# Performance work log

Measured on AMD Instinct MI355X. Metric: run time of the kernel, lower is better.

The kernel has to match this reference:

```python
import jax, jax.numpy as jnp
import numpy as np

B, N, DIM, H, HD, COND, BS = 2, 1024, 768, 12, 64, 128, 16
S = 2 * N  # noised tokens [0:N) concatenated with clean x0 tokens [N:2N)
EPS = 1e-5
NEG = -1e30


def setup_inputs() -> dict:
    key = jax.random.key(0)
    ks = jax.random.split(key, 8)
    d = {}
    d['x'] = jax.random.normal(ks[0], (B, S, DIM), jnp.float32)
    d['c'] = jax.random.normal(ks[1], (B, COND), jnp.float32)
    # Rotary table for positions 0..N-1 (each half of the 2N sequence reuses the same positions)
    inv_freq = 1.0 / (10000.0 ** (np.arange(0, HD, 2, dtype=np.float64) / HD))
    freqs = np.arange(N, dtype=np.float64)[:, None] * inv_freq[None, :]
    emb = np.concatenate([freqs, freqs], axis=-1)  # [N, HD]
    cos = np.tile(np.cos(emb), (2, 1))[None, :, None, None, :]
    sin = np.tile(np.sin(emb), (2, 1))[None, :, None, None, :]
    d['cos'] = jnp.asarray(cos, jnp.float32)
    d['sin'] = jnp.asarray(sin, jnp.float32)
    # block-causal diffusion mask (flex_attention_mask): same (block, x0-flag) OR
    # cross-attention from noised block q>0 to strictly earlier CLEAN (x0) blocks
    idx = np.arange(S)
    fl = (idx >= N).astype(np.int64)
    blk = np.where(fl == 1, (idx - N) // BS, idx // BS)
    same = (blk[:, None] == blk[None, :]) & (fl[:, None] == fl[None, :])
    allowed = (blk[:, None] > 0) & (blk[None, :] < blk[:, None]) & (fl[None, :] == 1)
    d['mask'] = jnp.asarray(same | allowed)
    # parameters (adaLN is zero-init in the source; randomized here so the block is non-trivial)
    w = 0.02
    d['norm1_w'] = jnp.ones((DIM,), jnp.float32)
    d['qkv_w'] = jax.random.normal(ks[2], (3 * DIM, DIM), jnp.float32) * w
    d['attn_out_w'] = jax.random.normal(ks[3], (DIM, DIM), jnp.float32) * w
    d['norm2_w'] = jnp.ones((DIM,), jnp.float32)
    d['mlp_w1'] = jax.random.normal(ks[4], (4 * DIM, DIM), jnp.float32) * w
    d['mlp_b1'] = jnp.zeros((4 * DIM,), jnp.float32)
    d['mlp_w2'] = jax.random.normal(ks[5], (DIM, 4 * DIM), jnp.float32) * w
    d['mlp_b2'] = jnp.zeros((DIM,), jnp.float32)
    d['adaLN_w'] = jax.random.normal(ks[6], (6 * DIM, COND), jnp.float32) * w
    d['adaLN_b'] = jax.random.normal(ks[7], (6 * DIM,), jnp.float32) * w
    return d


def _ln(x, w):
    # F.layer_norm (no bias) followed by learned scale, as in the custom LayerNorm
    mu = x.mean(-1, keepdims=True)
    xc = x - mu
    var = (xc * xc).mean(-1, keepdims=True)
    return xc * jax.lax.rsqrt(var + EPS) * w


def reference(x, c, cos, sin, mask, norm1_w, qkv_w, attn_out_w, norm2_w,
              mlp_w1, mlp_b1, mlp_w2, mlp_b2, adaLN_w, adaLN_b):
    # adaLN modulation: [B, 6*DIM] -> six [B, 1, DIM] chunks
    mods = c @ adaLN_w.T + adaLN_b
    (shift_msa, scale_msa, gate_msa,
     shift_mlp, scale_mlp, gate_mlp) = jnp.split(mods[:, None, :], 6, axis=-1)
    x_skip = x
    h = _ln(x, norm1_w) * (1.0 + scale_msa) + shift_msa  # modulate_fused
    # qkv projection + rotary (torchscript path: qkv*cos + rotate_half(qkv)*sin)
    qkv = (h @ qkv_w.T).reshape(x.shape[0], S, 3, H, HD)
    rot = jnp.concatenate([-qkv[..., HD // 2:], qkv[..., :HD // 2]], axis=-1)
    qkv = qkv * cos + rot * sin
    q, k, v = qkv[:, :, 0], qkv[:, :, 1], qkv[:, :, 2]
    # SDPA with the block-causal diffusion mask, scale 1/sqrt(head_dim)
    scores = jnp.einsum('bqhd,bkhd->bhqk', q, k) / np.sqrt(HD).astype(np.float32)
    scores = jnp.where(mask[None, None], scores, NEG)
    p = jax.nn.softmax(scores, axis=-1)
    a = jnp.einsum('bhqk,bkhd->bqhd', p, v).reshape(x.shape[0], S, DIM)
    # bias_dropout_add_scale (inference => no dropout): gate * attn_out + residual
    x = gate_msa * (a @ attn_out_w.T) + x_skip
    h2 = _ln(x, norm2_w) * (1.0 + scale_mlp) + shift_mlp
    m = jax.nn.gelu(h2 @ mlp_w1.T + mlp_b1, approximate=True) @ mlp_w2.T + mlp_b2
    return x + gate_mlp * m
```

## Files before the change

kernel.cpp:

```cpp
#include <hip/hip_runtime.h>
#include <hip/hip_bf16.h>

#define EPS 1e-5f

typedef __attribute__((ext_vector_type(8))) short bf16x8;
typedef __attribute__((ext_vector_type(4))) short bf16x4;
typedef __attribute__((ext_vector_type(4))) float f32x4;

__device__ __forceinline__ f32x4 mfma_bf16(bf16x8 a, bf16x8 b, f32x4 c) {
    return __builtin_amdgcn_mfma_f32_16x16x32_bf16(a, b, c, 0, 0, 0);
}

__device__ __forceinline__ void async_ld16(const void* g, void* l) {
    __builtin_amdgcn_global_load_lds(
        (const __attribute__((address_space(1))) void*)g,
        (__attribute__((address_space(3))) void*)l, 16, 0, 0);
}

__device__ __forceinline__ float fast_gelu(float v) {
    float z2 = 1.5957691216057308f * (v + 0.044715f * v * v * v);
    float e = __expf(z2);
    return v * e / (e + 1.f);
}

__device__ __forceinline__ float bf2f(short s) {
    union { float f; unsigned u; } v;
    v.u = ((unsigned)(unsigned short)s) << 16;
    return v.f;
}

__global__ void k_pre(const float* __restrict__ a, __hip_bfloat16* __restrict__ oa, int na,
                      const float* __restrict__ b, __hip_bfloat16* __restrict__ ob, int nb,
                      const float* __restrict__ c, __hip_bfloat16* __restrict__ oc, int nc,
                      const float* __restrict__ d, __hip_bfloat16* __restrict__ od, int nd,
                      const float* __restrict__ cond, const float* __restrict__ alw,
                      const float* __restrict__ alb, float* __restrict__ mods) {
    if (blockIdx.x >= 27648) {
        int i = (blockIdx.x - 27648) * 256 + threadIdx.x;
        int bb = i / 4608, row = i - bb * 4608;
        const float4* cv = (const float4*)(cond + bb * 128);
        const float4* wv = (const float4*)(alw + (long)row * 128);
        float acc = 0.f;
#pragma unroll
        for (int k = 0; k < 32; ++k) {
            float4 x = cv[k], y = wv[k];
            acc += x.x * y.x + x.y * y.y + x.z * y.z + x.w * y.w;
        }
        mods[i] = acc + alb[row];
        return;
    }
    int i = blockIdx.x * 256 + threadIdx.x;
    if (i < na) { oa[i] = __float2bfloat16(a[i]); return; }
    i -= na;
    if (i < nb) { ob[i] = __float2bfloat16(b[i]); return; }
    i -= nb;
    if (i < nc) { oc[i] = __float2bfloat16(c[i]); return; }
    i -= nc;
    if (i < nd) od[i] = __float2bfloat16(d[i]);
}

__global__ void k_ln_mod(const float* __restrict__ x, const float* __restrict__ w,
                         const float* __restrict__ mods, int shiftOff, int scaleOff,
                         __hip_bfloat16* __restrict__ out) {
    int token = blockIdx.x;
    int lane = threadIdx.x;
    const float4* xr = (const float4*)(x + (long)token * 768);
    float4 v0 = xr[lane], v1 = xr[lane + 64], v2 = xr[lane + 128];
    float s  = v0.x + v0.y + v0.z + v0.w + v1.x + v1.y + v1.z + v1.w + v2.x + v2.y + v2.z + v2.w;
    float ss = v0.x*v0.x + v0.y*v0.y + v0.z*v0.z + v0.w*v0.w
             + v1.x*v1.x + v1.y*v1.y + v1.z*v1.z + v1.w*v1.w
             + v2.x*v2.x + v2.y*v2.y + v2.z*v2.z + v2.w*v2.w;
#pragma unroll
    for (int m = 32; m >= 1; m >>= 1) { s += __shfl_xor(s, m); ss += __shfl_xor(ss, m); }
    float mu = s * (1.f / 768.f);
    float var = ss * (1.f / 768.f) - mu * mu;
    float rs = rsqrtf(var + EPS);
    int b = token >> 11;
    const float* sh = mods + b * 4608 + shiftOff;
    const float* sc = mods + b * 4608 + scaleOff;
    __hip_bfloat16* o = out + (long)token * 768;
    float4 vv[3] = {v0, v1, v2};
#pragma unroll
    for (int kk = 0; kk < 3; ++kk) {
        int cbase = (lane + 64 * kk) * 4;
        const float* p = (const float*)&vv[kk];
#pragma unroll
        for (int j = 0; j < 4; ++j) {
            int col = cbase + j;
            float hv = (p[j] - mu) * rs * w[col] * (1.f + sc[col]) + sh[col];
            o[col] = __float2bfloat16(hv);
        }
    }
}

__global__ void k_red(const __hip_bfloat16* __restrict__ p, const float* __restrict__ x2,
                      const float* __restrict__ mods, const float* __restrict__ bias,
                      float* __restrict__ out) {
    long base = ((long)blockIdx.x * 256 + threadIdx.x) * 4;
    int col = (int)(base % 768);
    int row = (int)(base / 768);
    int b = row >> 11;
    short4 a0 = *(const short4*)(p + base);
    short4 a1 = *(const short4*)(p + 3145728 + base);
    float4 xr = *(const float4*)(x2 + base);
    float4 gt = *(const float4*)(mods + b * 4608 + 3840 + col);
    float4 bs = *(const float4*)(bias + col);
    float4 o;
    o.x = xr.x + gt.x * (bf2f(a0.x) + bf2f(a1.x) + bs.x);
    o.y = xr.y + gt.y * (bf2f(a0.y) + bf2f(a1.y) + bs.y);
    o.z = xr.z + gt.z * (bf2f(a0.z) + bf2f(a1.z) + bs.z);
    o.w = xr.w + gt.w * (bf2f(a0.w) + bf2f(a1.w) + bs.w);
    *(float4*)(out + base) = o;
}

__global__ __launch_bounds__(64) void k_attn(
    const __hip_bfloat16* __restrict__ q, const __hip_bfloat16* __restrict__ k,
    const __hip_bfloat16* __restrict__ vT, __hip_bfloat16* __restrict__ out) {
    __shared__ __hip_bfloat16 P[640];
    int lane = threadIdx.x;
    int l15 = lane & 15, quad = lane >> 4;
    int idx = blockIdx.x;
    int bh = idx % 24;
    int r = idx / 24;
    int fl, blk;
    if (r & 1) { fl = 1; blk = 63 - (r >> 1); }
    else       { fl = 0; blk = 63 - (r >> 1); }
    int qblk = fl * 64 + blk;

    const __hip_bfloat16* Q = q + ((long)bh * 2048 + qblk * 16) * 64;
    bf16x8 qa = *(const bf16x8*)(Q + l15 * 64 + quad * 8);
    bf16x8 qb = *(const bf16x8*)(Q + l15 * 64 + 32 + quad * 8);
    const __hip_bfloat16* K = k + (long)bh * 2048 * 64;
    const __hip_bfloat16* V = vT + (long)bh * 64 * 2048;

    const f32x4 vzero = {0.f, 0.f, 0.f, 0.f};
    f32x4 o[4]; float l[4];
#pragma unroll
    for (int rr = 0; rr < 4; ++rr) { o[rr] = vzero; l[rr] = 0.f; }

    int plen = (blk + fl) * 16;
    int nch = (plen + 31) >> 5;
    int total = nch + (fl ? 0 : 1);

    int kbase = (0 < nch) ? 1024 : blk * 16;
    bool v1 = (0 < nch) && (16 < plen);
    bf16x8 ka, kb, k1a, k1b;
    {
        const __hip_bfloat16* K0 = K + (long)kbase * 64;
        ka = *(const bf16x8*)(K0 + l15 * 64 + quad * 8);
        kb = *(const bf16x8*)(K0 + l15 * 64 + 32 + quad * 8);
        k1a = ka; k1b = kb;
        if (v1) {
            const __hip_bfloat16* K1 = K0 + 16 * 64;
            k1a = *(const bf16x8*)(K1 + l15 * 64 + quad * 8);
            k1b = *(const bf16x8*)(K1 + l15 * 64 + 32 + quad * 8);
        }
    }

    for (int ci = 0; ci < total; ++ci) {
        bf16x8 vf[4];
#pragma unroll
        for (int tt = 0; tt < 4; ++tt)
            vf[tt] = *(const bf16x8*)(V + (long)(tt * 16 + l15) * 2048 + kbase + quad * 8);

        f32x4 s0 = mfma_bf16(qb, kb, mfma_bf16(qa, ka, vzero));
        f32x4 s1 = vzero;
        if (v1) s1 = mfma_bf16(qb, k1b, mfma_bf16(qa, k1a, vzero));

        bool hasNext = (ci + 1) < total;
        int nkbase = kbase; bool nv1 = false;
        bf16x8 nka = ka, nkb = kb, nk1a = ka, nk1b = kb;
        if (hasNext) {
            nkbase = (ci + 1 < nch) ? 1024 + (ci + 1) * 32 : blk * 16;
            nv1 = (ci + 1 < nch) && ((ci + 1) * 32 + 16) < plen;
            const __hip_bfloat16* K0 = K + (long)nkbase * 64;
            nka = *(const bf16x8*)(K0 + l15 * 64 + quad * 8);
            nkb = *(const bf16x8*)(K0 + l15 * 64 + 32 + quad * 8);
            if (nv1) {
                const __hip_bfloat16* K1 = K0 + 16 * 64;
                nk1a = *(const bf16x8*)(K1 + l15 * 64 + quad * 8);
                nk1b = *(const bf16x8*)(K1 + l15 * 64 + 32 + quad * 8);
            }
        }

        float p0[4], p1[4];
#pragma unroll
        for (int rr = 0; rr < 4; ++rr) p0[rr] = __expf(s0[rr]);
        if (v1) {
#pragma unroll
            for (int rr = 0; rr < 4; ++rr) p1[rr] = __expf(s1[rr]);
        } else {
#pragma unroll
            for (int rr = 0; rr < 4; ++rr) p1[rr] = 0.f;
        }
#pragma unroll
        for (int rr = 0; rr < 4; ++rr) {
            l[rr] += p0[rr] + p1[rr];
            int row = quad * 4 + rr;
            P[row * 36 + l15]      = __float2bfloat16(p0[rr]);
            P[row * 36 + 16 + l15] = __float2bfloat16(p1[rr]);
        }
        asm volatile("s_waitcnt lgkmcnt(0)" ::: "memory");
        union { bf16x4 h[2]; bf16x8 v; } u;
        u.h[0] = *(const bf16x4*)(P + l15 * 36 + quad * 8);
        u.h[1] = *(const bf16x4*)(P + l15 * 36 + quad * 8 + 4);
        bf16x8 pa = u.v;
#pragma unroll
        for (int tt = 0; tt < 4; ++tt) o[tt] = mfma_bf16(pa, vf[tt], o[tt]);
        asm volatile("s_waitcnt lgkmcnt(0)" ::: "memory");

        kbase = nkbase; v1 = nv1;
        ka = nka; kb = nkb; k1a = nk1a; k1b = nk1b;
    }

    int b = bh / 12, h = bh - b * 12;
    int seqbase = qblk * 16;
#pragma unroll
    for (int rr = 0; rr < 4; ++rr) {
        float lr = l[rr];
#pragma unroll
        for (int msk = 1; msk < 16; msk <<= 1) lr += __shfl_xor(lr, msk, 16);
        float inv = 1.f / lr;
        long row = b * 2048 + seqbase + quad * 4 + rr;
#pragma unroll
        for (int tt = 0; tt < 4; ++tt)
            out[row * 768 + h * 64 + tt * 16 + l15] = __float2bfloat16(o[tt][rr] * inv);
    }
}

template <int MODE, int TN>
__global__ __launch_bounds__(TN == 128 ? 256 : 128) void k_gemm(
    const __hip_bfloat16* __restrict__ A, const __hip_bfloat16* __restrict__ W,
    float* __restrict__ Cf, __hip_bfloat16* __restrict__ Cb,
    const float* __restrict__ bias, const float* __restrict__ mods, int gateOff,
    const float* __restrict__ resid, const float* __restrict__ cosb,
    const float* __restrict__ sinb, __hip_bfloat16* __restrict__ qo,
    __hip_bfloat16* __restrict__ ko, __hip_bfloat16* __restrict__ vo,
    int M, int N, int K, int lda) {
    constexpr int NW = (TN == 128) ? 4 : 2;
    constexpr int ACH = 512 / (NW * 64);
    constexpr int BCH = (TN * 4) / (NW * 64);
    constexpr int NINST = ACH + BCH;
    __shared__ __hip_bfloat16 lA[2][128 * 32];
    __shared__ __hip_bfloat16 lB[2][TN * 32];
    int t = threadIdx.x;
    int wave = t >> 6, lane = t & 63, l15 = lane & 15, quad = lane >> 4;
    int wr = (TN == 128) ? (wave >> 1) : wave;
    int wc = (TN == 128) ? (wave & 1) : 0;
    int sw8 = (quad ^ ((l15 >> 1) & 3)) * 8;
    long bm = blockIdx.x, bn = blockIdx.y;
    const __hip_bfloat16* Ab = A + bm * 128 * lda + (long)blockIdx.z * K;
    const __hip_bfloat16* Wb = W + bn * TN * lda + (long)blockIdx.z * K;

    long soffA[ACH], soffB[BCH];
#pragma unroll
    for (int cc = 0; cc < ACH; ++cc) {
        int chunk = cc * NW * 64 + t;
        int row = chunk >> 2;
        int c = (chunk & 3) ^ ((row >> 1) & 3);
        soffA[cc] = (long)row * lda + c * 8;
    }
#pragma unroll
    for (int cc = 0; cc < BCH; ++cc) {
        int chunk = cc * NW * 64 + t;
        int row = chunk >> 2;
        int c = (chunk & 3) ^ ((row >> 1) & 3);
        soffB[cc] = (long)row * lda + c * 8;
    }
    auto stage = [&](int k0, int buf) {
        char* lAc = (char*)&lA[buf][0];
        char* lBc = (char*)&lB[buf][0];
#pragma unroll
        for (int cc = 0; cc < ACH; ++cc)
            async_ld16(Ab + soffA[cc] + k0, lAc + cc * (NW * 1024) + wave * 1024);
#pragma unroll
        for (int cc = 0; cc < BCH; ++cc)
            async_ld16(Wb + soffB[cc] + k0, lBc + cc * (NW * 1024) + wave * 1024);
    };

    f32x4 acc[4][4];
#pragma unroll
    for (int i = 0; i < 4; ++i)
#pragma unroll
        for (int j = 0; j < 4; ++j) acc[i][j] = (f32x4){0.f, 0.f, 0.f, 0.f};

    int nIter = K / 32;
    stage(0, 0);
    for (int i = 0; i < nIter; ++i) {
        int cb = i & 1;
        if (i > 0) asm volatile("s_barrier" ::: "memory");
        if (i + 1 < nIter) {
            stage((i + 1) * 32, cb ^ 1);
            asm volatile("s_waitcnt vmcnt(%0)" :: "n"(NINST) : "memory");
        } else {
            asm volatile("s_waitcnt vmcnt(0)" ::: "memory");
        }
        asm volatile("s_barrier" ::: "memory");
        bf16x8 af[4], bfr[4];
#pragma unroll
        for (int ii = 0; ii < 4; ++ii)
            af[ii] = *(const bf16x8*)&lA[cb][(wr * 64 + ii * 16 + l15) * 32 + sw8];
#pragma unroll
        for (int j = 0; j < 4; ++j)
            bfr[j] = *(const bf16x8*)&lB[cb][(wc * 64 + j * 16 + l15) * 32 + sw8];
#pragma unroll
        for (int ii = 0; ii < 4; ++ii)
#pragma unroll
            for (int j = 0; j < 4; ++j)
                acc[ii][j] = mfma_bf16(af[ii], bfr[j], acc[ii][j]);
    }

    if (MODE == 4) {
        int hcol = (int)bn * 2 + wc;
        int th = hcol / 12, h = hcol % 12;
#pragma unroll
        for (int i = 0; i < 4; ++i) {
#pragma unroll
            for (int r = 0; r < 4; ++r) {
                int row = (int)bm * 128 + wr * 64 + i * 16 + quad * 4 + r;
                int s = row & 2047, b = row >> 11;
                long bh_ = b * 12 + h;
                const float* cbp = cosb + s * 64;
                const float* sbp = sinb + s * 64;
#pragma unroll
                for (int j = 0; j < 2; ++j) {
                    int dh = j * 16 + l15;
                    float a0f = acc[i][j][r], a1f = acc[i][j + 2][r];
                    float o0 = a0f * cbp[dh] - a1f * sbp[dh];
                    float o1 = a1f * cbp[dh + 32] + a0f * sbp[dh + 32];
                    if (th == 0) {
                        __hip_bfloat16* d = qo + (bh_ * 2048 + s) * 64;
                        d[dh]      = __float2bfloat16(o0 * 0.125f);
                        d[dh + 32] = __float2bfloat16(o1 * 0.125f);
                    } else if (th == 1) {
                        __hip_bfloat16* d = ko + (bh_ * 2048 + s) * 64;
                        d[dh]      = __float2bfloat16(o0);
                        d[dh + 32] = __float2bfloat16(o1);
                    } else {
                        __hip_bfloat16* d = vo + bh_ * 64 * 2048 + s;
                        d[(long)dh * 2048]        = __float2bfloat16(o0);
                        d[(long)(dh + 32) * 2048] = __float2bfloat16(o1);
                    }
                }
            }
        }
        return;
    }

#pragma unroll
    for (int i = 0; i < 4; ++i) {
#pragma unroll
        for (int j = 0; j < 4; ++j) {
#pragma unroll
            for (int r = 0; r < 4; ++r) {
                int row = (int)bm * 128 + wr * 64 + i * 16 + quad * 4 + r;
                int col = (int)bn * TN + wc * 64 + j * 16 + l15;
                float v = acc[i][j][r];
                long idx = (long)row * N + col;
                if (MODE == 1) {
                    Cf[idx] = mods[(row >> 11) * 4608 + gateOff + col] * v + resid[idx];
                } else if (MODE == 2) {
                    Cb[idx] = __float2bfloat16(fast_gelu(v + bias[col]));
                } else if (MODE == 3) {
                    Cf[idx] = resid[idx] + mods[(row >> 11) * 4608 + gateOff + col] * (v + bias[col]);
                } else {
                    Cb[(long)blockIdx.z * M * N + idx] = __float2bfloat16(v);
                }
            }
        }
    }
}

extern "C" void kernel_launch(void* const* d_in, const int* in_sizes, int n_in,
                              void* d_out, int out_size, void* d_ws, size_t ws_size,
                              hipStream_t stream) {
    const float* x    = (const float*)d_in[0];
    const float* c    = (const float*)d_in[1];
    const float* cosb = (const float*)d_in[2];
    const float* sinb = (const float*)d_in[3];
    const float* n1w  = (const float*)d_in[5];
    const float* qkvw = (const float*)d_in[6];
    const float* aow  = (const float*)d_in[7];
    const float* n2w  = (const float*)d_in[8];
    const float* w1   = (const float*)d_in[9];
    const float* b1   = (const float*)d_in[10];
    const float* w2   = (const float*)d_in[11];
    const float* b2   = (const float*)d_in[12];
    const float* alw  = (const float*)d_in[13];
    const float* alb  = (const float*)d_in[14];

    char* ws = (char*)d_ws;
    size_t off = 0;
    auto alloc = [&](size_t bytes) -> void* {
        void* p = ws + off;
        off += (bytes + 255) & ~(size_t)255;
        return p;
    };
    float*          mods = (float*)alloc(2 * 4608 * 4);
    __hip_bfloat16* hbuf = (__hip_bfloat16*)alloc((size_t)4096 * 768 * 2);
    __hip_bfloat16* qb   = (__hip_bfloat16*)alloc((size_t)24 * 2048 * 64 * 2);
    __hip_bfloat16* kb   = (__hip_bfloat16*)alloc((size_t)24 * 2048 * 64 * 2);
    __hip_bfloat16* vT   = (__hip_bfloat16*)alloc((size_t)24 * 64 * 2048 * 2);
    __hip_bfloat16* abuf = (__hip_bfloat16*)alloc((size_t)4096 * 768 * 2);
    float*          x2   = (float*)alloc((size_t)4096 * 768 * 4);
    __hip_bfloat16* h2   = (__hip_bfloat16*)alloc((size_t)4096 * 768 * 2);
    __hip_bfloat16* m1   = (__hip_bfloat16*)alloc((size_t)4096 * 3072 * 2);
    __hip_bfloat16* m2p  = (__hip_bfloat16*)alloc((size_t)2 * 4096 * 768 * 2);
    __hip_bfloat16* wq   = (__hip_bfloat16*)alloc((size_t)2304 * 768 * 2);
    __hip_bfloat16* wa   = (__hip_bfloat16*)alloc((size_t)768 * 768 * 2);
    __hip_bfloat16* w1b  = (__hip_bfloat16*)alloc((size_t)3072 * 768 * 2);
    __hip_bfloat16* w2b  = (__hip_bfloat16*)alloc((size_t)768 * 3072 * 2);

    k_pre<<<27684, 256, 0, stream>>>(qkvw, wq, 2304 * 768, aow, wa, 768 * 768,
                                     w1, w1b, 3072 * 768, w2, w2b, 768 * 3072,
                                     c, alw, alb, mods);
    k_ln_mod<<<4096, 64, 0, stream>>>(x, n1w, mods, 0, 768, hbuf);
    k_gemm<4, 128><<<dim3(32, 18), 256, 0, stream>>>(hbuf, wq, nullptr, nullptr, nullptr, nullptr, 0,
                                                     nullptr, cosb, sinb, qb, kb, vT,
                                                     4096, 2304, 768, 768);
    k_attn<<<3072, 64, 0, stream>>>(qb, kb, vT, abuf);
    k_gemm<1, 64><<<dim3(32, 12), 128, 0, stream>>>(abuf, wa, x2, nullptr, nullptr, mods, 1536,
                                                    x, nullptr, nullptr, nullptr, nullptr, nullptr,
                                                    4096, 768, 768, 768);
    k_ln_mod<<<4096, 64, 0, stream>>>(x2, n2w, mods, 2304, 3072, h2);
    k_gemm<2, 128><<<dim3(32, 24), 256, 0, stream>>>(h2, w1b, nullptr, m1, b1, nullptr, 0,
                                                     nullptr, nullptr, nullptr, nullptr, nullptr, nullptr,
                                                     4096, 3072, 768, 768);
    k_gemm<5, 128><<<dim3(32, 6, 2), 256, 0, stream>>>(m1, w2b, nullptr, m2p, nullptr, nullptr, 0,
                                                       nullptr, nullptr, nullptr, nullptr, nullptr, nullptr,
                                                       4096, 768, 1536, 3072);
    k_red<<<3072, 256, 0, stream>>>(m2p, x2, mods, b2, (float*)d_out);
}
```

Baseline: 316.4 us.

## Process four 16-key tiles per attention iteration with per-tile key gathering

The attention loop now handles up to four 16-key tiles per iteration instead of a 32-key chunk, addressing each tile independently. The clean-prefix tiles and the diagonal self-block can therefore share one iteration, and the V fragments are gathered per tile. This cuts loop iterations, LDS round-trips and barriers per key, and gives the scheduler more independent MFMAs to overlap, at the cost of higher register use and wasted work on inactive padding tiles.

```diff
diff --git a/kernel.cpp b/kernel.cpp
--- a/kernel.cpp
+++ b/kernel.cpp
@@ -116,7 +116,7 @@
 __global__ __launch_bounds__(64) void k_attn(
     const __hip_bfloat16* __restrict__ q, const __hip_bfloat16* __restrict__ k,
     const __hip_bfloat16* __restrict__ vT, __hip_bfloat16* __restrict__ out) {
-    __shared__ __hip_bfloat16 P[640];
+    __shared__ __hip_bfloat16 P[16 * 68];
     int lane = threadIdx.x;
     int l15 = lane & 15, quad = lane >> 4;
     int idx = blockIdx.x;
@@ -139,78 +139,88 @@
     for (int rr = 0; rr < 4; ++rr) { o[rr] = vzero; l[rr] = 0.f; }
 
     int plen = (blk + fl) * 16;
-    int nch = (plen + 31) >> 5;
-    int total = nch + (fl ? 0 : 1);
-
-    int kbase = (0 < nch) ? 1024 : blk * 16;
-    bool v1 = (0 < nch) && (16 < plen);
-    bf16x8 ka, kb, k1a, k1b;
-    {
-        const __hip_bfloat16* K0 = K + (long)kbase * 64;
-        ka = *(const bf16x8*)(K0 + l15 * 64 + quad * 8);
-        kb = *(const bf16x8*)(K0 + l15 * 64 + 32 + quad * 8);
-        k1a = ka; k1b = kb;
-        if (v1) {
-            const __hip_bfloat16* K1 = K0 + 16 * 64;
-            k1a = *(const bf16x8*)(K1 + l15 * 64 + quad * 8);
-            k1b = *(const bf16x8*)(K1 + l15 * 64 + 32 + quad * 8);
-        }
-    }
-
-    for (int ci = 0; ci < total; ++ci) {
-        bf16x8 vf[4];
-#pragma unroll
-        for (int tt = 0; tt < 4; ++tt)
-            vf[tt] = *(const bf16x8*)(V + (long)(tt * 16 + l15) * 2048 + kbase + quad * 8);
-
-        f32x4 s0 = mfma_bf16(qb, kb, mfma_bf16(qa, ka, vzero));
-        f32x4 s1 = vzero;
-        if (v1) s1 = mfma_bf16(qb, k1b, mfma_bf16(qa, k1a, vzero));
-
-        bool hasNext = (ci + 1) < total;
-        int nkbase = kbase; bool nv1 = false;
-        bf16x8 nka = ka, nkb = kb, nk1a = ka, nk1b = kb;
-        if (hasNext) {
-            nkbase = (ci + 1 < nch) ? 1024 + (ci + 1) * 32 : blk * 16;
-            nv1 = (ci + 1 < nch) && ((ci + 1) * 32 + 16) < plen;
-            const __hip_bfloat16* K0 = K + (long)nkbase * 64;
-            nka = *(const bf16x8*)(K0 + l15 * 64 + quad * 8);
-            nkb = *(const bf16x8*)(K0 + l15 * 64 + 32 + quad * 8);
-            if (nv1) {
-                const __hip_bfloat16* K1 = K0 + 16 * 64;
-                nk1a = *(const bf16x8*)(K1 + l15 * 64 + quad * 8);
-                nk1b = *(const bf16x8*)(K1 + l15 * 64 + 32 + quad * 8);
+    int pre = plen >> 4;
+    int total16 = pre + (fl ? 0 : 1);
+    int nIter = (total16 + 3) >> 2;
+
+    auto stBase = [&](int t, bool act) -> int {
+        return act ? ((t < pre) ? 1024 + t * 16 : blk * 16) : 0;
+    };
+
+    int st[4]; bool act[4];
+    bf16x8 ka[4], kb8[4];
+#pragma unroll
+    for (int s = 0; s < 4; ++s) {
+        act[s] = s < total16;
+        st[s] = stBase(s, act[s]);
+        const __hip_bfloat16* K0 = K + (long)st[s] * 64;
+        ka[s]  = *(const bf16x8*)(K0 + l15 * 64 + quad * 8);
+        kb8[s] = *(const bf16x8*)(K0 + l15 * 64 + 32 + quad * 8);
+    }
+
+    for (int ci = 0; ci < nIter; ++ci) {
+        bf16x8 vf[2][4];
+#pragma unroll
+        for (int p2 = 0; p2 < 2; ++p2) {
+            int kbv_lo = st[2 * p2], kbv_hi = st[2 * p2 + 1];
+            int kbv = (quad < 2) ? kbv_lo : kbv_hi;
+            int inner = (quad & 1) * 8;
+#pragma unroll
+            for (int tt = 0; tt < 4; ++tt)
+                vf[p2][tt] = *(const bf16x8*)(V + (long)(tt * 16 + l15) * 2048 + kbv + inner);
+        }
+
+        f32x4 sc[4];
+#pragma unroll
+        for (int s = 0; s < 4; ++s)
+            sc[s] = mfma_bf16(qb, kb8[s], mfma_bf16(qa, ka[s], vzero));
+
+        int nst[4]; bool nact[4];
+        bf16x8 nka[4], nkb[4];
+        if (ci + 1 < nIter) {
+#pragma unroll
+            for (int s = 0; s < 4; ++s) {
+                int t = 4 * (ci + 1) + s;
+                nact[s] = t < total16;
+                nst[s] = stBase(t, nact[s]);
+                const __hip_bfloat16* K0 = K + (long)nst[s] * 64;
+                nka[s] = *(const bf16x8*)(K0 + l15 * 64 + quad * 8);
+                nkb[s] = *(const bf16x8*)(K0 + l15 * 64 + 32 + quad * 8);
             }
         }
 
-        float p0[4], p1[4];
-#pragma unroll
-        for (int rr = 0; rr < 4; ++rr) p0[rr] = __expf(s0[rr]);
-        if (v1) {
-#pragma unroll
-            for (int rr = 0; rr < 4; ++rr) p1[rr] = __expf(s1[rr]);
-        } else {
-#pragma unroll
-            for (int rr = 0; rr < 4; ++rr) p1[rr] = 0.f;
-        }
-#pragma unroll
-        for (int rr = 0; rr < 4; ++rr) {
-            l[rr] += p0[rr] + p1[rr];
-            int row = quad * 4 + rr;
-            P[row * 36 + l15]      = __float2bfloat16(p0[rr]);
-            P[row * 36 + 16 + l15] = __float2bfloat16(p1[rr]);
+#pragma unroll
+        for (int s = 0; s < 4; ++s) {
+#pragma unroll
+            for (int rr = 0; rr < 4; ++rr) {
+                float pv = act[s] ? __expf(sc[s][rr]) : 0.f;
+                l[rr] += pv;
+                P[(quad * 4 + rr) * 68 + s * 16 + l15] = __float2bfloat16(pv);
+            }
         }
         asm volatile("s_waitcnt lgkmcnt(0)" ::: "memory");
-        union { bf16x4 h[2]; bf16x8 v; } u;
-        u.h[0] = *(const bf16x4*)(P + l15 * 36 + quad * 8);
-        u.h[1] = *(const bf16x4*)(P + l15 * 36 + quad * 8 + 4);
-        bf16x8 pa = u.v;
-#pragma unroll
-        for (int tt = 0; tt < 4; ++tt) o[tt] = mfma_bf16(pa, vf[tt], o[tt]);
+        bf16x8 pa[2];
+#pragma unroll
+        for (int p2 = 0; p2 < 2; ++p2) {
+            union { bf16x4 h[2]; bf16x8 v; } u;
+            u.h[0] = *(const bf16x4*)(P + l15 * 68 + p2 * 32 + quad * 8);
+            u.h[1] = *(const bf16x4*)(P + l15 * 68 + p2 * 32 + quad * 8 + 4);
+            pa[p2] = u.v;
+        }
         asm volatile("s_waitcnt lgkmcnt(0)" ::: "memory");
-
-        kbase = nkbase; v1 = nv1;
-        ka = nka; kb = nkb; k1a = nk1a; k1b = nk1b;
+#pragma unroll
+        for (int p2 = 0; p2 < 2; ++p2)
+#pragma unroll
+            for (int tt = 0; tt < 4; ++tt)
+                o[tt] = mfma_bf16(pa[p2], vf[p2][tt], o[tt]);
+
+        if (ci + 1 < nIter) {
+#pragma unroll
+            for (int s = 0; s < 4; ++s) {
+                st[s] = nst[s]; act[s] = nact[s];
+                ka[s] = nka[s]; kb8[s] = nkb[s];
+            }
+        }
     }
 
     int b = bh / 12, h = bh - b * 12;
```

Result: no change. 314.4 us (-0.6%).
